# Performance work log

Hardware: AMD Instinct MI355X
Metric: run time of the kernel (lower is better)

## Reference

```python
import jax, jax.numpy as jnp
import numpy as np

HIDDEN = 1024
HEADS = 16
HEAD_DIM = HIDDEN // HEADS


def setup_inputs() -> dict:
    key = jax.random.key(0)
    ks = jax.random.split(key, 9)
    B, S = 2, 2048
    std = 1.0 / np.sqrt(HIDDEN)
    inp = {
        'hidden_states': jax.random.normal(ks[0], (B, S, HIDDEN), dtype=jnp.float32),
        'attention_mask': jnp.ones((B, S), dtype=jnp.int32),
        'wq': jax.random.normal(ks[1], (HIDDEN, HIDDEN), dtype=jnp.float32) * std,
        'bq': jnp.zeros((HIDDEN,), dtype=jnp.float32),
        'wk': jax.random.normal(ks[2], (HIDDEN, HIDDEN), dtype=jnp.float32) * std,
        'bk': jnp.zeros((HIDDEN,), dtype=jnp.float32),
        'wv': jax.random.normal(ks[3], (HIDDEN, HIDDEN), dtype=jnp.float32) * std,
        'bv': jnp.zeros((HIDDEN,), dtype=jnp.float32),
        'wo': jax.random.normal(ks[4], (HIDDEN, HIDDEN), dtype=jnp.float32) * std,
        'bo': jnp.zeros((HIDDEN,), dtype=jnp.float32),
    }
    return inp


def reference(hidden_states, attention_mask, wq, bq, wk, bk, wv, bv, wo, bo):
    B, S, H = hidden_states.shape
    def heads(x):  # [B,S,H] -> [B,nh,S,hd]
        return x.reshape(B, S, HEADS, HEAD_DIM).transpose(0, 2, 1, 3)
    q = heads(hidden_states @ wq + bq)
    k = heads(hidden_states @ wk + bk)
    v = heads(hidden_states @ wv + bv)
    scores = jnp.einsum('bhqd,bhkd->bhqk', q, k) / np.sqrt(HEAD_DIM).astype(np.float32)
    causal = jnp.tril(jnp.ones((S, S), dtype=bool))  # True = keep
    keep = causal[None, None] & (attention_mask[:, None, None, :] != 0)
    scores = jnp.where(keep, scores, -jnp.inf)
    probs = jax.nn.softmax(scores, axis=-1)
    out = jnp.einsum('bhqk,bhkd->bhqd', probs, v)  # [B,nh,S,hd]
    out = out.transpose(0, 2, 1, 3).reshape(B, S, H)
    return out @ wo + bo
```

## Files before the change

kernel.cpp:

```cpp
#include <hip/hip_runtime.h>

#define HID   1024
#define SLEN  2048
#define NHEAD 16
#define HDIM  64
#define SC2L  0.18033688f

typedef unsigned short u16;
typedef _Float16 f16;
using bf16x8 = __attribute__((ext_vector_type(8))) short;
using h16x2  = __attribute__((ext_vector_type(2))) __fp16;
using f16x4  = __attribute__((ext_vector_type(4))) f16;
using f32x4  = __attribute__((ext_vector_type(4))) float;

typedef __attribute__((address_space(1))) void gvoid;
typedef __attribute__((address_space(3))) void lvoid;

__device__ __forceinline__ u16 f2bf(float f) {
  union { float f; unsigned u; } v; v.f = f;
  unsigned u = v.u;
  return (u16)((u + 0x7fffu + ((u >> 16) & 1u)) >> 16);
}

__device__ __forceinline__ void async_ld16(const u16* g, u16* l) {
  __builtin_amdgcn_global_load_lds((gvoid*)g, (lvoid*)l, 16, 0, 0);
}

__global__ __launch_bounds__(256) void prep_kernel(const float* __restrict__ x,
                                                   const float* __restrict__ wq,
                                                   const float* __restrict__ wk,
                                                   const float* __restrict__ wv,
                                                   const float* __restrict__ wo,
                                                   u16* __restrict__ xb,
                                                   u16* __restrict__ wt) {
  const int tid = threadIdx.x;
  if (blockIdx.z == 4) {
    const int bid = blockIdx.y * 32 + blockIdx.x;
#pragma unroll
    for (int it = 0; it < 4; ++it) {
      const int i = bid * 1024 + it * 256 + tid;
      float4 v = ((const float4*)x)[i];
      ushort4 o;
      o.x = f2bf(v.x); o.y = f2bf(v.y); o.z = f2bf(v.z); o.w = f2bf(v.w);
      ((ushort4*)xb)[i] = o;
    }
    return;
  }
  const float* src = (blockIdx.z == 0) ? wq : (blockIdx.z == 1) ? wk
                   : (blockIdx.z == 2) ? wv : wo;
  u16* dst = wt + (size_t)blockIdx.z * (HID * HID);
  __shared__ float tile[32][33];
  const int n0 = blockIdx.x * 32, k0 = blockIdx.y * 32;
  const int xx = tid & 31, yy = tid >> 5;
  for (int i = yy; i < 32; i += 8)
    tile[i][xx] = src[(size_t)(k0 + i) * HID + n0 + xx];
  __syncthreads();
  for (int i = yy; i < 32; i += 8)
    dst[(size_t)(n0 + i) * HID + k0 + xx] = f2bf(tile[xx][i]);
}

__global__ __launch_bounds__(256) void gemm_qkv_kernel(const u16* __restrict__ A,
                                                       const u16* __restrict__ Bt,
                                                       const float* __restrict__ bq,
                                                       const float* __restrict__ bk,
                                                       const float* __restrict__ bv,
                                                       u16* __restrict__ Qb,
                                                       u16* __restrict__ Kb,
                                                       u16* __restrict__ VTf) {
  __shared__ u16 smem[16384];
  const int tid  = threadIdx.x;
  const int wave = tid >> 6, lane = tid & 63;
  const int quad = lane >> 4, l16 = lane & 15;
  const int raw = blockIdx.y * 24 + blockIdx.x;
  const int logi = (raw & 7) * 96 + (raw >> 3);
  const int bx = logi % 24, by = logi / 24;
  const int n0g = bx * 128;
  const int region = bx >> 3;
  const int colbase = (bx & 7) * 128;
  const int m0 = by * 128;
  const int wm = (wave & 1) * 64, wn = (wave >> 1) * 64;

  f32x4 acc[4][4] = {};
  const int srow = lane >> 2;
  const int scol = (lane & 3) * 8;

#define STAGE_G(kt, bi)                                                          \
  for (int c = wave; c < 8; c += 4) {                                            \
    async_ld16(A  + (size_t)(m0  + c * 16 + srow) * HID + (kt) + scol,           \
               &smem[(bi) * 8192 + c * 512]);                                    \
    async_ld16(Bt + (size_t)(n0g + c * 16 + srow) * HID + (kt) + scol,           \
               &smem[(bi) * 8192 + 4096 + c * 512]);                             \
  }

  STAGE_G(0, 0);
  for (int ks = 0; ks < 32; ++ks) {
    const int bi = ks & 1;
    if (ks < 31) {
      STAGE_G((ks + 1) * 32, bi ^ 1);
      asm volatile("s_waitcnt vmcnt(4)" ::: "memory");
    } else {
      asm volatile("s_waitcnt vmcnt(0)" ::: "memory");
    }
    __builtin_amdgcn_s_barrier();

    const u16* sA = smem + bi * 8192;
    const u16* sB = smem + bi * 8192 + 4096;
    bf16x8 af[4], bfr[4];
#pragma unroll
    for (int t = 0; t < 4; ++t) {
      af[t]  = *(const bf16x8*)&sA[(wm + t * 16 + l16) * 32 + quad * 8];
      bfr[t] = *(const bf16x8*)&sB[(wn + t * 16 + l16) * 32 + quad * 8];
    }
#pragma unroll
    for (int mt = 0; mt < 4; ++mt)
#pragma unroll
      for (int nt = 0; nt < 4; ++nt)
        acc[mt][nt] = __builtin_amdgcn_mfma_f32_16x16x32_bf16(af[mt], bfr[nt],
                                                              acc[mt][nt], 0, 0, 0);
    __builtin_amdgcn_s_barrier();
  }
#undef STAGE_G

  const float* bias = (region == 0) ? bq : (region == 1) ? bk : bv;
  float bvv[4];
#pragma unroll
  for (int nt = 0; nt < 4; ++nt) bvv[nt] = bias[colbase + wn + nt * 16 + l16];

  if (region == 2) {
    const int bb = m0 >> 11;
    const int m0loc = m0 & 2047;
    const int h0 = colbase >> 6;
    u16* T = smem;
#pragma unroll
    for (int h2 = 0; h2 < 2; ++h2) {
      __syncthreads();
      if ((wave >> 1) == h2) {
#pragma unroll
        for (int mt = 0; mt < 4; ++mt)
#pragma unroll
          for (int nt = 0; nt < 4; ++nt)
#pragma unroll
            for (int r = 0; r < 4; ++r) {
              const int sl = (wave & 1) * 64 + mt * 16 + quad * 4 + r;
              const int dl = nt * 16 + l16;
              union { f16 h; u16 u; } cv;
              cv.h = (f16)(acc[mt][nt][r] + bvv[nt]);
              T[dl * 128 + (((sl >> 3) ^ l16) * 8) + (sl & 7)] = cv.u;
            }
      }
      __syncthreads();
      const int d = tid >> 2, sg = (tid & 3) * 4;
      u16* slab0 = VTf + ((size_t)((bb * NHEAD + h0 + h2) * 128 + (m0loc >> 4))) * 1024;
#pragma unroll
      for (int cc = 0; cc < 4; ++cc) {
        const int cl = sg + cc;
        const int ph = cl ^ (d & 15);
        const int slot = (d * 2 + (cl & 1)) ^ ((d >> 2) & 1);
        *(bf16x8*)(slab0 + (size_t)(cl >> 1) * 1024 + slot * 8)
            = *(const bf16x8*)&T[d * 128 + ph * 8];
      }
    }
    return;
  }

  u16* C = (region == 0) ? Qb : Kb;
#pragma unroll
  for (int mt = 0; mt < 4; ++mt)
#pragma unroll
    for (int r = 0; r < 4; ++r) {
      const int row = m0 + wm + mt * 16 + quad * 4 + r;
#pragma unroll
      for (int nt = 0; nt < 4; ++nt) {
        const int col = colbase + wn + nt * 16 + l16;
        C[(size_t)row * HID + col] = f2bf(acc[mt][nt][r] + bvv[nt]);
      }
    }
}

__global__ __launch_bounds__(256) void gemm_o_kernel(const u16* __restrict__ A,
                                                     const u16* __restrict__ Bt,
                                                     const float* __restrict__ bias,
                                                     float* __restrict__ Cf) {
  __shared__ u16 smem[12288];
  const int tid  = threadIdx.x;
  const int wave = tid >> 6, lane = tid & 63;
  const int quad = lane >> 4, l16 = lane & 15;
  const int raw = blockIdx.y * 8 + blockIdx.x;
  const int logi = (raw & 7) * 64 + (raw >> 3);
  const int n0 = (logi & 7) * 128;
  const int m0 = (logi >> 3) * 64;
  const int wn = wave * 32;

  f32x4 acc[4][2] = {};
  const int srow = lane >> 2;
  const int scol = (lane & 3) * 8;

#define STAGE_O(kt, bi)                                                          \
  for (int c = wave; c < 12; c += 4) {                                           \
    if (c < 4) async_ld16(A + (size_t)(m0 + c * 16 + srow) * HID + (kt) + scol,  \
                          &smem[(bi) * 6144 + c * 512]);                         \
    else async_ld16(Bt + (size_t)(n0 + (c - 4) * 16 + srow) * HID + (kt) + scol, \
                    &smem[(bi) * 6144 + 2048 + (c - 4) * 512]);                  \
  }

  STAGE_O(0, 0);
  for (int ks = 0; ks < 32; ++ks) {
    const int bi = ks & 1;
    if (ks < 31) {
      STAGE_O((ks + 1) * 32, bi ^ 1);
      asm volatile("s_waitcnt vmcnt(3)" ::: "memory");
    } else {
      asm volatile("s_waitcnt vmcnt(0)" ::: "memory");
    }
    __builtin_amdgcn_s_barrier();

    const u16* sA = smem + bi * 6144;
    const u16* sB = smem + bi * 6144 + 2048;
    bf16x8 af[4], bfr[2];
#pragma unroll
    for (int t = 0; t < 4; ++t)
      af[t] = *(const bf16x8*)&sA[(t * 16 + l16) * 32 + quad * 8];
#pragma unroll
    for (int t = 0; t < 2; ++t)
      bfr[t] = *(const bf16x8*)&sB[(wn + t * 16 + l16) * 32 + quad * 8];
#pragma unroll
    for (int mt = 0; mt < 4; ++mt)
#pragma unroll
      for (int nt = 0; nt < 2; ++nt)
        acc[mt][nt] = __builtin_amdgcn_mfma_f32_16x16x32_bf16(af[mt], bfr[nt],
                                                              acc[mt][nt], 0, 0, 0);
    __builtin_amdgcn_s_barrier();
  }
#undef STAGE_O

  float bvv[2];
#pragma unroll
  for (int nt = 0; nt < 2; ++nt) bvv[nt] = bias[n0 + wn + nt * 16 + l16];
#pragma unroll
  for (int mt = 0; mt < 4; ++mt)
#pragma unroll
    for (int r = 0; r < 4; ++r) {
      const int row = m0 + mt * 16 + quad * 4 + r;
#pragma unroll
      for (int nt = 0; nt < 2; ++nt)
        Cf[(size_t)row * HID + n0 + wn + nt * 16 + l16] = acc[mt][nt][r] + bvv[nt];
    }
}

__global__ __launch_bounds__(256, 2) void flash_attn_kernel(const u16* __restrict__ Q,
                                                            const u16* __restrict__ K,
                                                            const u16* __restrict__ VT,
                                                            const int* __restrict__ mask,
                                                            u16* __restrict__ O) {
  const int id = blockIdx.x;
  const int t_ = id >> 8;
  const int u_ = (id >> 5) & 7;
  const int bh = id & 31;
  const int h  = bh & 15, b = bh >> 4;
  const int qt = (t_ == 0) ? u_ : (t_ == 1) ? (15 - u_)
               : (t_ == 2) ? (16 + u_) : (31 - u_);
  const int tid  = threadIdx.x;
  const int wave = tid >> 6, lane = tid & 63;
  const int quad = lane >> 4, l16 = lane & 15;

  __shared__ alignas(16) char smraw[35840];
  u16*   Ks  = (u16*)smraw;
  u16*   Vt  = (u16*)(smraw + 16384);
  float* Ob0 = (float*)smraw;
  float* Ob1 = (float*)(smraw + 16896);
  float* lb  = (float*)(smraw + 33792);

  const u16* Kh  = K  + (size_t)b * SLEN * HID + h * HDIM;
  const u16* Vth = VT + (size_t)(b * NHEAD + h) * (128 * 1024);

  const int srow8 = lane >> 3;
  const int gch   = (lane & 7) ^ srow8;
  const int rx    = l16 & 7;

  unsigned mw = 0;
  {
    const int4* mrow = (const int4*)(mask + b * SLEN);
#pragma unroll
    for (int c = 0; c < 8; ++c) {
      int4 m = mrow[lane * 8 + c];
      mw |= (m.x ? 1u : 0u) << (c * 4);
      mw |= (m.y ? 1u : 0u) << (c * 4 + 1);
      mw |= (m.z ? 1u : 0u) << (c * 4 + 2);
      mw |= (m.w ? 1u : 0u) << (c * 4 + 3);
    }
  }
  const int mb = (wave & 1) * 16 + quad * 4;

  const int q0 = qt * 64;

  bf16x8 qb_[4][2];
#pragma unroll
  for (int nt = 0; nt < 4; ++nt) {
    const u16* qp = Q + (size_t)(b * SLEN + q0 + nt * 16 + l16) * HID + h * HDIM + quad * 8;
    qb_[nt][0] = *(const bf16x8*)qp;
    qb_[nt][1] = *(const bf16x8*)(qp + 32);
  }

  f32x4 oacc[4][4] = {};
  float l_part[4] = {0.f, 0.f, 0.f, 0.f};

  const int r0s = wave * 16 + srow8;
#define STAGE_KV(jt, bufi)                                                      \
  {                                                                             \
    u16* kd = Ks + (bufi) * 4096 + wave * 1024;                                 \
    async_ld16(Kh + (size_t)((jt) * 64 + r0s) * HID + gch * 8,       kd);       \
    async_ld16(Kh + (size_t)((jt) * 64 + r0s + 8) * HID + gch * 8,   kd + 512); \
    const u16* vs = Vth + (size_t)((jt) * 4 + wave) * 1024;                     \
    u16* vd = Vt + (bufi) * 4096 + wave * 1024;                                 \
    async_ld16(vs + lane * 8,        vd);                                       \
    async_ld16(vs + (64 + lane) * 8, vd + 512);                                 \
  }

  STAGE_KV(0, 0);

  for (int j = 0; j <= qt; ++j) {
    const int buf = j & 1;
    u16* KsB = Ks + buf * 4096;
    u16* VtB = Vt + buf * 4096;

    if (j < qt) {
      STAGE_KV(j + 1, buf ^ 1);
      asm volatile("s_waitcnt vmcnt(6)" ::: "memory");
    } else {
      asm volatile("s_waitcnt vmcnt(2)" ::: "memory");
    }

    const unsigned wbits = __shfl(mw, 2 * j + (wave >> 1));
    float map[4];
#pragma unroll
    for (int r = 0; r < 4; ++r)
      map[r] = ((wbits >> (mb + r)) & 1u) ? 0.f : -1e30f;

    const u16* kp = KsB + (wave * 16 + l16) * 64;
    const int ph0 = quad ^ rx;
    const bf16x8 ka0 = *(const bf16x8*)(kp + ph0 * 8);
    const bf16x8 ka1 = *(const bf16x8*)(kp + (ph0 ^ 4) * 8);

    float p_[4][4];
#pragma unroll
    for (int nt = 0; nt < 4; ++nt) {
      f32x4 z = {0.f, 0.f, 0.f, 0.f};
      z = __builtin_amdgcn_mfma_f32_16x16x32_bf16(ka0, qb_[nt][0], z, 0, 0, 0);
      z = __builtin_amdgcn_mfma_f32_16x16x32_bf16(ka1, qb_[nt][1], z, 0, 0, 0);
#pragma unroll
      for (int r = 0; r < 4; ++r)
        p_[nt][r] = exp2f(fmaf(z[r], SC2L, map[r]));
    }
    if (j == qt) {
#pragma unroll
      for (int nt = 0; nt < 4; ++nt)
#pragma unroll
        for (int r = 0; r < 4; ++r)
          if (wave * 16 + quad * 4 + r > nt * 16 + l16) p_[nt][r] = 0.f;
    }

    f16x4 pb[4];
#pragma unroll
    for (int nt = 0; nt < 4; ++nt) {
      l_part[nt] += (p_[nt][0] + p_[nt][1]) + (p_[nt][2] + p_[nt][3]);
      union { h16x2 h[2]; f16x4 v; } u;
      u.h[0] = __builtin_amdgcn_cvt_pkrtz(p_[nt][0], p_[nt][1]);
      u.h[1] = __builtin_amdgcn_cvt_pkrtz(p_[nt][2], p_[nt][3]);
      pb[nt] = u.v;
    }

    if (j < qt) {
      asm volatile("s_waitcnt vmcnt(4)" ::: "memory");
    } else {
      asm volatile("s_waitcnt vmcnt(0)" ::: "memory");
    }

#pragma unroll
    for (int dt = 0; dt < 4; ++dt) {
      const int dd = dt * 16 + l16;
      const int slot = (dd * 2 + (quad >> 1)) ^ ((dd >> 2) & 1);
      const f16x4 va = *(const f16x4*)(VtB + wave * 1024 + slot * 8 + (quad & 1) * 4);
#pragma unroll
      for (int nt = 0; nt < 4; ++nt)
        oacc[dt][nt] = __builtin_amdgcn_mfma_f32_16x16x16f16(va, pb[nt], oacc[dt][nt], 0, 0, 0);
    }
  }
#undef STAGE_KV

  __syncthreads();

#pragma unroll
  for (int nt = 0; nt < 4; ++nt) {
    l_part[nt] += __shfl_xor(l_part[nt], 16);
    l_part[nt] += __shfl_xor(l_part[nt], 32);
  }
  if (quad == 0)
#pragma unroll
    for (int nt = 0; nt < 4; ++nt) lb[wave * 64 + nt * 16 + l16] = l_part[nt];

  if ((wave & 1) == 0) {
    float* ob = (wave == 0) ? Ob0 : Ob1;
#pragma unroll
    for (int dt = 0; dt < 4; ++dt)
#pragma unroll
      for (int nt = 0; nt < 4; ++nt)
#pragma unroll
        for (int r = 0; r < 4; ++r)
          ob[(dt * 16 + quad * 4 + r) * 66 + nt * 16 + l16] = oacc[dt][nt][r];
  }
  __syncthreads();
  if (wave & 1) {
    float* ob = (wave == 1) ? Ob0 : Ob1;
#pragma unroll
    for (int dt = 0; dt < 4; ++dt)
#pragma unroll
      for (int nt = 0; nt < 4; ++nt)
#pragma unroll
        for (int r = 0; r < 4; ++r)
          ob[(dt * 16 + quad * 4 + r) * 66 + nt * 16 + l16] += oacc[dt][nt][r];
  }
  __syncthreads();

  {
    const int q  = tid >> 2;
    const int dc = tid & 3;
    const float l = lb[q] + lb[64 + q] + lb[128 + q] + lb[192 + q];
    const float inv = 1.f / l;
    u16 ob[16];
#pragma unroll
    for (int e = 0; e < 16; ++e) {
      const int d = dc * 16 + e;
      ob[e] = f2bf((Ob0[d * 66 + q] + Ob1[d * 66 + q]) * inv);
    }
    u16* op = O + (size_t)(b * SLEN + q0 + q) * HID + h * HDIM + dc * 16;
    *(bf16x8*)op       = *(bf16x8*)&ob[0];
    *(bf16x8*)(op + 8) = *(bf16x8*)&ob[8];
  }
}

extern "C" void kernel_launch(void* const* d_in, const int* in_sizes, int n_in,
                              void* d_out, int out_size, void* d_ws, size_t ws_size,
                              hipStream_t stream) {
  const float* x    = (const float*)d_in[0];
  const int*   mask = (const int*)d_in[1];
  const float* wq   = (const float*)d_in[2];
  const float* bq   = (const float*)d_in[3];
  const float* wk   = (const float*)d_in[4];
  const float* bk   = (const float*)d_in[5];
  const float* wv   = (const float*)d_in[6];
  const float* bv   = (const float*)d_in[7];
  const float* wo   = (const float*)d_in[8];
  const float* bo   = (const float*)d_in[9];
  float* out = (float*)d_out;

  char* ws = (char*)d_ws;
  u16* XBF = (u16*)(ws);
  u16* WT  = (u16*)(ws + (8u  << 20));
  u16* QBF = (u16*)(ws + (16u << 20));
  u16* KBF = (u16*)(ws + (24u << 20));
  u16* VTF = (u16*)(ws + (32u << 20));
  u16* ATT = (u16*)(ws);

  prep_kernel<<<dim3(32, 32, 5), 256, 0, stream>>>(x, wq, wk, wv, wo, XBF, WT);
  gemm_qkv_kernel<<<dim3(24, 32), 256, 0, stream>>>(XBF, WT, bq, bk, bv, QBF, KBF, VTF);
  flash_attn_kernel<<<dim3(1024), 256, 0, stream>>>(QBF, KBF, VTF, mask, ATT);
  gemm_o_kernel<<<dim3(8, 64), 256, 0, stream>>>(ATT, WT + (3u << 20), bo, out);
}
```

Baseline: 195.0 us.

## Load K/V fragments directly from global into registers with register double-buffering

Replaces the async global-to-LDS staging of K and V tiles, and the subsequent LDS reads, with direct per-lane global loads into register fragments. The loop is manually unrolled by two so the next tile's registers prefetch while the current tile computes. This removes LDS traffic and wait-count management. In exchange it uses more registers and issues less coalesced global loads, with each wave reading its own strided K rows straight from L2.

New measurement: 199.6 us. +2.4%, slower.

```diff
diff --git a/kernel.cpp b/kernel.cpp
--- a/kernel.cpp
+++ b/kernel.cpp
@@ -263,19 +263,13 @@
   const int wave = tid >> 6, lane = tid & 63;
   const int quad = lane >> 4, l16 = lane & 15;
 
-  __shared__ alignas(16) char smraw[35840];
-  u16*   Ks  = (u16*)smraw;
-  u16*   Vt  = (u16*)(smraw + 16384);
+  __shared__ alignas(16) char smraw[34816];
   float* Ob0 = (float*)smraw;
   float* Ob1 = (float*)(smraw + 16896);
   float* lb  = (float*)(smraw + 33792);
 
   const u16* Kh  = K  + (size_t)b * SLEN * HID + h * HDIM;
   const u16* Vth = VT + (size_t)(b * NHEAD + h) * (128 * 1024);
-
-  const int srow8 = lane >> 3;
-  const int gch   = (lane & 7) ^ srow8;
-  const int rx    = l16 & 7;
 
   unsigned mw = 0;
   {
@@ -304,49 +298,39 @@
   f32x4 oacc[4][4] = {};
   float l_part[4] = {0.f, 0.f, 0.f, 0.f};
 
-  const int r0s = wave * 16 + srow8;
-#define STAGE_KV(jt, bufi)                                                      \
-  {                                                                             \
-    u16* kd = Ks + (bufi) * 4096 + wave * 1024;                                 \
-    async_ld16(Kh + (size_t)((jt) * 64 + r0s) * HID + gch * 8,       kd);       \
-    async_ld16(Kh + (size_t)((jt) * 64 + r0s + 8) * HID + gch * 8,   kd + 512); \
-    const u16* vs = Vth + (size_t)((jt) * 4 + wave) * 1024;                     \
-    u16* vd = Vt + (bufi) * 4096 + wave * 1024;                                 \
-    async_ld16(vs + lane * 8,        vd);                                       \
-    async_ld16(vs + (64 + lane) * 8, vd + 512);                                 \
-  }
-
-  STAGE_KV(0, 0);
-
-  for (int j = 0; j <= qt; ++j) {
-    const int buf = j & 1;
-    u16* KsB = Ks + buf * 4096;
-    u16* VtB = Vt + buf * 4096;
-
-    if (j < qt) {
-      STAGE_KV(j + 1, buf ^ 1);
-      asm volatile("s_waitcnt vmcnt(6)" ::: "memory");
-    } else {
-      asm volatile("s_waitcnt vmcnt(2)" ::: "memory");
-    }
-
+  const u16* kbase = Kh + (size_t)(wave * 16 + l16) * HID + quad * 8;
+  int voff[4];
+#pragma unroll
+  for (int dt = 0; dt < 4; ++dt) {
+    const int dd = dt * 16 + l16;
+    const int slot = (dd * 2 + (quad >> 1)) ^ ((dd >> 2) & 1);
+    voff[dt] = slot * 8 + (quad & 1) * 4;
+  }
+  const u16* vbase = Vth + wave * 1024;
+
+  auto LOADKV = [&](int j, bf16x8& k0, bf16x8& k1, f16x4* v) {
+    const u16* kp = kbase + (size_t)j * 64 * HID;
+    k0 = *(const bf16x8*)kp;
+    k1 = *(const bf16x8*)(kp + 32);
+    const u16* vp = vbase + j * 4096;
+#pragma unroll
+    for (int dt = 0; dt < 4; ++dt)
+      v[dt] = *(const f16x4*)(vp + voff[dt]);
+  };
+
+  auto BODY = [&](int j, const bf16x8& k0, const bf16x8& k1, const f16x4* v) {
     const unsigned wbits = __shfl(mw, 2 * j + (wave >> 1));
     float map[4];
 #pragma unroll
     for (int r = 0; r < 4; ++r)
       map[r] = ((wbits >> (mb + r)) & 1u) ? 0.f : -1e30f;
 
-    const u16* kp = KsB + (wave * 16 + l16) * 64;
-    const int ph0 = quad ^ rx;
-    const bf16x8 ka0 = *(const bf16x8*)(kp + ph0 * 8);
-    const bf16x8 ka1 = *(const bf16x8*)(kp + (ph0 ^ 4) * 8);
-
     float p_[4][4];
 #pragma unroll
     for (int nt = 0; nt < 4; ++nt) {
       f32x4 z = {0.f, 0.f, 0.f, 0.f};
-      z = __builtin_amdgcn_mfma_f32_16x16x32_bf16(ka0, qb_[nt][0], z, 0, 0, 0);
-      z = __builtin_amdgcn_mfma_f32_16x16x32_bf16(ka1, qb_[nt][1], z, 0, 0, 0);
+      z = __builtin_amdgcn_mfma_f32_16x16x32_bf16(k0, qb_[nt][0], z, 0, 0, 0);
+      z = __builtin_amdgcn_mfma_f32_16x16x32_bf16(k1, qb_[nt][1], z, 0, 0, 0);
 #pragma unroll
       for (int r = 0; r < 4; ++r)
         p_[nt][r] = exp2f(fmaf(z[r], SC2L, map[r]));
@@ -363,29 +347,31 @@
 #pragma unroll
     for (int nt = 0; nt < 4; ++nt) {
       l_part[nt] += (p_[nt][0] + p_[nt][1]) + (p_[nt][2] + p_[nt][3]);
-      union { h16x2 h[2]; f16x4 v; } u;
-      u.h[0] = __builtin_amdgcn_cvt_pkrtz(p_[nt][0], p_[nt][1]);
-      u.h[1] = __builtin_amdgcn_cvt_pkrtz(p_[nt][2], p_[nt][3]);
-      pb[nt] = u.v;
-    }
-
-    if (j < qt) {
-      asm volatile("s_waitcnt vmcnt(4)" ::: "memory");
-    } else {
-      asm volatile("s_waitcnt vmcnt(0)" ::: "memory");
-    }
-
-#pragma unroll
-    for (int dt = 0; dt < 4; ++dt) {
-      const int dd = dt * 16 + l16;
-      const int slot = (dd * 2 + (quad >> 1)) ^ ((dd >> 2) & 1);
-      const f16x4 va = *(const f16x4*)(VtB + wave * 1024 + slot * 8 + (quad & 1) * 4);
+      union { h16x2 hh[2]; f16x4 vv; } u;
+      u.hh[0] = __builtin_amdgcn_cvt_pkrtz(p_[nt][0], p_[nt][1]);
+      u.hh[1] = __builtin_amdgcn_cvt_pkrtz(p_[nt][2], p_[nt][3]);
+      pb[nt] = u.vv;
+    }
+
+#pragma unroll
+    for (int dt = 0; dt < 4; ++dt)
 #pragma unroll
       for (int nt = 0; nt < 4; ++nt)
-        oacc[dt][nt] = __builtin_amdgcn_mfma_f32_16x16x16f16(va, pb[nt], oacc[dt][nt], 0, 0, 0);
-    }
-  }
-#undef STAGE_KV
+        oacc[dt][nt] = __builtin_amdgcn_mfma_f32_16x16x16f16(v[dt], pb[nt], oacc[dt][nt], 0, 0, 0);
+  };
+
+  bf16x8 kA0, kA1, kB0, kB1;
+  f16x4  vA[4], vB[4];
+  LOADKV(0, kA0, kA1, vA);
+  int j = 0;
+  for (;;) {
+    if (j < qt) LOADKV(j + 1, kB0, kB1, vB);
+    BODY(j, kA0, kA1, vA);
+    if (++j > qt) break;
+    if (j < qt) LOADKV(j + 1, kA0, kA1, vA);
+    BODY(j, kB0, kB1, vB);
+    if (++j > qt) break;
+  }
 
   __syncthreads();
 
```

## Share K/V tiles across two query tiles per 512-thread attention block

Applied to the files above, without the earlier changes.

The flash attention kernel now launches 512-thread blocks, each covering 128 queries as two 64-query halves that share the K/V tiles staged in LDS. K and V loading is split between the two halves of the block, and staging moves to a triple-buffered ring with a block barrier each iteration. Per-key mask words are loaded per tile instead of being bit-packed up front. This halves global K/V traffic per query, at the cost of a block-wide barrier every tile, idle iterations for the lower half on the diagonal, and more LDS per block, which may reduce occupancy.

Result: no change. 195.1 us (+0.1%).

```diff
diff --git a/kernel.cpp b/kernel.cpp
--- a/kernel.cpp
+++ b/kernel.cpp
@@ -247,28 +247,30 @@
     }
 }
 
-__global__ __launch_bounds__(256, 2) void flash_attn_kernel(const u16* __restrict__ Q,
-                                                            const u16* __restrict__ K,
-                                                            const u16* __restrict__ VT,
-                                                            const int* __restrict__ mask,
-                                                            u16* __restrict__ O) {
+__global__ __launch_bounds__(512) void flash_attn_kernel(const u16* __restrict__ Q,
+                                                         const u16* __restrict__ K,
+                                                         const u16* __restrict__ VT,
+                                                         const int* __restrict__ mask,
+                                                         u16* __restrict__ O) {
   const int id = blockIdx.x;
-  const int t_ = id >> 8;
+  const int t2 = id >> 8;
   const int u_ = (id >> 5) & 7;
   const int bh = id & 31;
   const int h  = bh & 15, b = bh >> 4;
-  const int qt = (t_ == 0) ? u_ : (t_ == 1) ? (15 - u_)
-               : (t_ == 2) ? (16 + u_) : (31 - u_);
+  const int qb2 = t2 ? (15 - u_) : u_;
   const int tid  = threadIdx.x;
   const int wave = tid >> 6, lane = tid & 63;
+  const int w4 = wave & 3, half = wave >> 2;
   const int quad = lane >> 4, l16 = lane & 15;
 
-  __shared__ alignas(16) char smraw[35840];
+  __shared__ alignas(16) char smraw[69632];
   u16*   Ks  = (u16*)smraw;
-  u16*   Vt  = (u16*)(smraw + 16384);
+  u16*   Vt  = (u16*)(smraw + 24576);
   float* Ob0 = (float*)smraw;
   float* Ob1 = (float*)(smraw + 16896);
-  float* lb  = (float*)(smraw + 33792);
+  float* Ob2 = (float*)(smraw + 33792);
+  float* Ob3 = (float*)(smraw + 50688);
+  float* lb  = (float*)(smraw + 67584);
 
   const u16* Kh  = K  + (size_t)b * SLEN * HID + h * HDIM;
   const u16* Vth = VT + (size_t)(b * NHEAD + h) * (128 * 1024);
@@ -277,21 +279,10 @@
   const int gch   = (lane & 7) ^ srow8;
   const int rx    = l16 & 7;
 
-  unsigned mw = 0;
-  {
-    const int4* mrow = (const int4*)(mask + b * SLEN);
-#pragma unroll
-    for (int c = 0; c < 8; ++c) {
-      int4 m = mrow[lane * 8 + c];
-      mw |= (m.x ? 1u : 0u) << (c * 4);
-      mw |= (m.y ? 1u : 0u) << (c * 4 + 1);
-      mw |= (m.z ? 1u : 0u) << (c * 4 + 2);
-      mw |= (m.w ? 1u : 0u) << (c * 4 + 3);
-    }
-  }
-  const int mb = (wave & 1) * 16 + quad * 4;
-
-  const int q0 = qt * 64;
+  const int nT = 2 * qb2 + 2;
+  const int dT = 2 * qb2 + half;
+
+  const int q0 = qb2 * 128 + half * 64;
 
   bf16x8 qb_[4][2];
 #pragma unroll
@@ -304,86 +295,88 @@
   f32x4 oacc[4][4] = {};
   float l_part[4] = {0.f, 0.f, 0.f, 0.f};
 
-  const int r0s = wave * 16 + srow8;
 #define STAGE_KV(jt, bufi)                                                      \
-  {                                                                             \
-    u16* kd = Ks + (bufi) * 4096 + wave * 1024;                                 \
-    async_ld16(Kh + (size_t)((jt) * 64 + r0s) * HID + gch * 8,       kd);       \
-    async_ld16(Kh + (size_t)((jt) * 64 + r0s + 8) * HID + gch * 8,   kd + 512); \
-    const u16* vs = Vth + (size_t)((jt) * 4 + wave) * 1024;                     \
-    u16* vd = Vt + (bufi) * 4096 + wave * 1024;                                 \
+  if (half == 0) {                                                              \
+    u16* kd = Ks + (bufi) * 4096 + w4 * 1024;                                   \
+    const u16* kp = Kh + (size_t)((jt) * 64 + w4 * 16 + srow8) * HID + gch * 8; \
+    async_ld16(kp,           kd);                                               \
+    async_ld16(kp + 8 * HID, kd + 512);                                         \
+  } else {                                                                      \
+    const u16* vs = Vth + (size_t)((jt) * 4 + w4) * 1024;                       \
+    u16* vd = Vt + (bufi) * 4096 + w4 * 1024;                                   \
     async_ld16(vs + lane * 8,        vd);                                       \
     async_ld16(vs + (64 + lane) * 8, vd + 512);                                 \
   }
 
   STAGE_KV(0, 0);
-
-  for (int j = 0; j <= qt; ++j) {
-    const int buf = j & 1;
-    u16* KsB = Ks + buf * 4096;
-    u16* VtB = Vt + buf * 4096;
-
-    if (j < qt) {
-      STAGE_KV(j + 1, buf ^ 1);
-      asm volatile("s_waitcnt vmcnt(6)" ::: "memory");
-    } else {
-      asm volatile("s_waitcnt vmcnt(2)" ::: "memory");
-    }
-
-    const unsigned wbits = __shfl(mw, 2 * j + (wave >> 1));
-    float map[4];
-#pragma unroll
-    for (int r = 0; r < 4; ++r)
-      map[r] = ((wbits >> (mb + r)) & 1u) ? 0.f : -1e30f;
-
-    const u16* kp = KsB + (wave * 16 + l16) * 64;
-    const int ph0 = quad ^ rx;
-    const bf16x8 ka0 = *(const bf16x8*)(kp + ph0 * 8);
-    const bf16x8 ka1 = *(const bf16x8*)(kp + (ph0 ^ 4) * 8);
-
-    float p_[4][4];
-#pragma unroll
-    for (int nt = 0; nt < 4; ++nt) {
-      f32x4 z = {0.f, 0.f, 0.f, 0.f};
-      z = __builtin_amdgcn_mfma_f32_16x16x32_bf16(ka0, qb_[nt][0], z, 0, 0, 0);
-      z = __builtin_amdgcn_mfma_f32_16x16x32_bf16(ka1, qb_[nt][1], z, 0, 0, 0);
-#pragma unroll
-      for (int r = 0; r < 4; ++r)
-        p_[nt][r] = exp2f(fmaf(z[r], SC2L, map[r]));
-    }
-    if (j == qt) {
-#pragma unroll
-      for (int nt = 0; nt < 4; ++nt)
-#pragma unroll
-        for (int r = 0; r < 4; ++r)
-          if (wave * 16 + quad * 4 + r > nt * 16 + l16) p_[nt][r] = 0.f;
-    }
-
-    f16x4 pb[4];
-#pragma unroll
-    for (int nt = 0; nt < 4; ++nt) {
-      l_part[nt] += (p_[nt][0] + p_[nt][1]) + (p_[nt][2] + p_[nt][3]);
-      union { h16x2 h[2]; f16x4 v; } u;
-      u.h[0] = __builtin_amdgcn_cvt_pkrtz(p_[nt][0], p_[nt][1]);
-      u.h[1] = __builtin_amdgcn_cvt_pkrtz(p_[nt][2], p_[nt][3]);
-      pb[nt] = u.v;
-    }
-
-    if (j < qt) {
-      asm volatile("s_waitcnt vmcnt(4)" ::: "memory");
+  int4 mi = *(const int4*)(mask + b * SLEN + w4 * 16 + quad * 4);
+
+  int cur = 0;
+  for (int j = 0; j < nT; ++j) {
+    int4 mi_n = mi;
+    if (j + 1 < nT) {
+      const int nb = (cur == 2) ? 0 : cur + 1;
+      STAGE_KV(j + 1, nb);
+      mi_n = *(const int4*)(mask + b * SLEN + (j + 1) * 64 + w4 * 16 + quad * 4);
+      asm volatile("s_waitcnt vmcnt(3)" ::: "memory");
     } else {
       asm volatile("s_waitcnt vmcnt(0)" ::: "memory");
     }
-
-#pragma unroll
-    for (int dt = 0; dt < 4; ++dt) {
-      const int dd = dt * 16 + l16;
-      const int slot = (dd * 2 + (quad >> 1)) ^ ((dd >> 2) & 1);
-      const f16x4 va = *(const f16x4*)(VtB + wave * 1024 + slot * 8 + (quad & 1) * 4);
-#pragma unroll
-      for (int nt = 0; nt < 4; ++nt)
-        oacc[dt][nt] = __builtin_amdgcn_mfma_f32_16x16x16f16(va, pb[nt], oacc[dt][nt], 0, 0, 0);
-    }
+    __builtin_amdgcn_s_barrier();
+
+    if (j <= dT) {
+      const u16* KsB = Ks + cur * 4096;
+      const u16* VtB = Vt + cur * 4096;
+
+      float map[4];
+      map[0] = mi.x ? 0.f : -1e30f;  map[1] = mi.y ? 0.f : -1e30f;
+      map[2] = mi.z ? 0.f : -1e30f;  map[3] = mi.w ? 0.f : -1e30f;
+
+      const u16* kp = KsB + (w4 * 16 + l16) * 64;
+      const int ph0 = quad ^ rx;
+      const bf16x8 ka0 = *(const bf16x8*)(kp + ph0 * 8);
+      const bf16x8 ka1 = *(const bf16x8*)(kp + (ph0 ^ 4) * 8);
+
+      float p_[4][4];
+#pragma unroll
+      for (int nt = 0; nt < 4; ++nt) {
+        f32x4 z = {0.f, 0.f, 0.f, 0.f};
+        z = __builtin_amdgcn_mfma_f32_16x16x32_bf16(ka0, qb_[nt][0], z, 0, 0, 0);
+        z = __builtin_amdgcn_mfma_f32_16x16x32_bf16(ka1, qb_[nt][1], z, 0, 0, 0);
+#pragma unroll
+        for (int r = 0; r < 4; ++r)
+          p_[nt][r] = exp2f(fmaf(z[r], SC2L, map[r]));
+      }
+      if (j == dT) {
+#pragma unroll
+        for (int nt = 0; nt < 4; ++nt)
+#pragma unroll
+          for (int r = 0; r < 4; ++r)
+            if (w4 * 16 + quad * 4 + r > nt * 16 + l16) p_[nt][r] = 0.f;
+      }
+
+      f16x4 pb[4];
+#pragma unroll
+      for (int nt = 0; nt < 4; ++nt) {
+        l_part[nt] += (p_[nt][0] + p_[nt][1]) + (p_[nt][2] + p_[nt][3]);
+        union { h16x2 hh[2]; f16x4 vv; } u;
+        u.hh[0] = __builtin_amdgcn_cvt_pkrtz(p_[nt][0], p_[nt][1]);
+        u.hh[1] = __builtin_amdgcn_cvt_pkrtz(p_[nt][2], p_[nt][3]);
+        pb[nt] = u.vv;
+      }
+
+#pragma unroll
+      for (int dt = 0; dt < 4; ++dt) {
+        const int dd = dt * 16 + l16;
+        const int slot = (dd * 2 + (quad >> 1)) ^ ((dd >> 2) & 1);
+        const f16x4 va = *(const f16x4*)(VtB + w4 * 1024 + slot * 8 + (quad & 1) * 4);
+#pragma unroll
+        for (int nt = 0; nt < 4; ++nt)
+          oacc[dt][nt] = __builtin_amdgcn_mfma_f32_16x16x16f16(va, pb[nt], oacc[dt][nt], 0, 0, 0);
+      }
+    }
+    mi = mi_n;
+    cur = (cur == 2) ? 0 : cur + 1;
   }
 #undef STAGE_KV
 
@@ -398,8 +391,9 @@
 #pragma unroll
     for (int nt = 0; nt < 4; ++nt) lb[wave * 64 + nt * 16 + l16] = l_part[nt];
 
-  if ((wave & 1) == 0) {
-    float* ob = (wave == 0) ? Ob0 : Ob1;
+  const int oi = half * 2 + (w4 >> 1);
+  float* ob = (oi == 0) ? Ob0 : (oi == 1) ? Ob1 : (oi == 2) ? Ob2 : Ob3;
+  if ((w4 & 1) == 0) {
 #pragma unroll
     for (int dt = 0; dt < 4; ++dt)
 #pragma unroll
@@ -409,8 +403,7 @@
           ob[(dt * 16 + quad * 4 + r) * 66 + nt * 16 + l16] = oacc[dt][nt][r];
   }
   __syncthreads();
-  if (wave & 1) {
-    float* ob = (wave == 1) ? Ob0 : Ob1;
+  if (w4 & 1) {
 #pragma unroll
     for (int dt = 0; dt < 4; ++dt)
 #pragma unroll
@@ -424,17 +417,21 @@
   {
     const int q  = tid >> 2;
     const int dc = tid & 3;
-    const float l = lb[q] + lb[64 + q] + lb[128 + q] + lb[192 + q];
+    const int hh = q >> 6, ql = q & 63;
+    const float l = lb[(hh * 4 + 0) * 64 + ql] + lb[(hh * 4 + 1) * 64 + ql]
+                  + lb[(hh * 4 + 2) * 64 + ql] + lb[(hh * 4 + 3) * 64 + ql];
     const float inv = 1.f / l;
-    u16 ob[16];
+    const float* obA = hh ? Ob2 : Ob0;
+    const float* obB = hh ? Ob3 : Ob1;
+    u16 obuf[16];
 #pragma unroll
     for (int e = 0; e < 16; ++e) {
       const int d = dc * 16 + e;
-      ob[e] = f2bf((Ob0[d * 66 + q] + Ob1[d * 66 + q]) * inv);
-    }
-    u16* op = O + (size_t)(b * SLEN + q0 + q) * HID + h * HDIM + dc * 16;
-    *(bf16x8*)op       = *(bf16x8*)&ob[0];
-    *(bf16x8*)(op + 8) = *(bf16x8*)&ob[8];
+      obuf[e] = f2bf((obA[d * 66 + ql] + obB[d * 66 + ql]) * inv);
+    }
+    u16* op = O + (size_t)(b * SLEN + qb2 * 128 + q) * HID + h * HDIM + dc * 16;
+    *(bf16x8*)op       = *(bf16x8*)&obuf[0];
+    *(bf16x8*)(op + 8) = *(bf16x8*)&obuf[8];
   }
 }
 
@@ -463,6 +460,6 @@
 
   prep_kernel<<<dim3(32, 32, 5), 256, 0, stream>>>(x, wq, wk, wv, wo, XBF, WT);
   gemm_qkv_kernel<<<dim3(24, 32), 256, 0, stream>>>(XBF, WT, bq, bk, bv, QBF, KBF, VTF);
-  flash_attn_kernel<<<dim3(1024), 256, 0, stream>>>(QBF, KBF, VTF, mask, ATT);
+  flash_attn_kernel<<<dim3(512), 512, 0, stream>>>(QBF, KBF, VTF, mask, ATT);
   gemm_o_kernel<<<dim3(8, 64), 256, 0, stream>>>(ATT, WT + (3u << 20), bo, out);
 }
```
